# Kernel optimization log

Hardware: AMD Instinct MI355X
Metric: run time of the kernel (lower is better)

## Reference

```python
import jax, jax.numpy as jnp
import numpy as np

N, D, V = 2048, 64, 2048


def setup_inputs() -> dict:
    key = jax.random.key(0)
    k_ids, k_emb, k_tree, k_map = jax.random.split(key, 4)
    language_ids = jax.random.randint(k_ids, (N,), 0, V)
    language_embeddings = jax.random.normal(k_emb, (N, D), dtype=jnp.float32)
    # symmetric distance tables, mimicking the symmetric try/except dict lookup
    t = jax.random.uniform(k_tree, (V, V), dtype=jnp.float32)
    tree_dist = (t + t.T) * 0.5
    m = jax.random.uniform(k_map, (V, V), dtype=jnp.float32)
    map_dist = (m + m.T) * 0.5
    return {
        "language_ids": language_ids,
        "language_embeddings": language_embeddings,
        "tree_dist": tree_dist,
        "map_dist": map_dist,
    }


def reference(language_ids, language_embeddings, tree_dist, map_dist):
    # pairwise mean-L1 distance between embeddings: [N, N]
    emb_dist = jnp.mean(
        jnp.abs(language_embeddings[:, None, :] - language_embeddings[None, :, :]),
        axis=-1,
    )
    # largest_value_map_dist as computed in __init__
    largest = jnp.max(map_dist)
    ii = language_ids[:, None]  # [N, 1]
    jj = language_ids[None, :]  # [1, N]
    metric = (tree_dist[ii, jj] + map_dist[ii, jj] / largest) * 0.5  # [N, N]
    # pairs with equal language ids are skipped in the original loop
    mask = (ii != jj).astype(emb_dist.dtype)
    per_pair = jnp.abs(emb_dist - metric) * mask
    return jnp.sum(per_pair) / jnp.sum(mask)
```

## Files before the change

kernel.cpp:

```cpp
#include <hip/hip_runtime.h>
#include <hip/hip_bf16.h>

#define NL 2048
#define DE 64
#define VV 2048
#define BT 32
#define NT (NL / BT)
#define NBLK (NT * (NT + 1) / 2)
#define STA 68
#define STB 36


__global__ __launch_bounds__(1024) void prep_kernel(const int* __restrict__ ids,
                                                    const float4* __restrict__ m4,
                                                    float* __restrict__ pmax,
                                                    int* __restrict__ perm,
                                                    int* __restrict__ sids) {
    const int t = threadIdx.x;
    const int lane = t & 63, wave = t >> 6;
    const int b = blockIdx.x;

    if (b < 256) {
        const float4* p = m4 + (size_t)b * 4096;
        const float4 x0 = p[t], x1 = p[t + 1024], x2 = p[t + 2048], x3 = p[t + 3072];
        float v = fmaxf(fmaxf(fmaxf(x0.x, x0.y), fmaxf(x0.z, x0.w)),
                        fmaxf(fmaxf(x1.x, x1.y), fmaxf(x1.z, x1.w)));
        v = fmaxf(v, fmaxf(fmaxf(x2.x, x2.y), fmaxf(x2.z, x2.w)));
        v = fmaxf(v, fmaxf(fmaxf(x3.x, x3.y), fmaxf(x3.z, x3.w)));
        #pragma unroll
        for (int o = 32; o > 0; o >>= 1)
            v = fmaxf(v, __shfl_down(v, o));
        __shared__ float wl[16];
        if (lane == 0) wl[wave] = v;
        __syncthreads();
        if (t == 0) {
            float m = wl[0];
            #pragma unroll
            for (int i = 1; i < 16; ++i) m = fmaxf(m, wl[i]);
            pmax[b] = m;
        }
    } else {
        __shared__ unsigned hist[VV];
        __shared__ unsigned offs[VV];
        __shared__ unsigned wtot[16];
        __shared__ unsigned wexc[16];
        hist[2 * t] = 0u; hist[2 * t + 1] = 0u;
        __syncthreads();
        const int id0 = ids[2 * t], id1 = ids[2 * t + 1];
        atomicAdd(&hist[id0], 1u);
        atomicAdd(&hist[id1], 1u);
        __syncthreads();
        const unsigned h0 = hist[2 * t], h1 = hist[2 * t + 1];
        const unsigned s = h0 + h1;
        unsigned ps = s;
        #pragma unroll
        for (int o = 1; o < 64; o <<= 1) {
            unsigned u = __shfl_up(ps, o);
            if (lane >= o) ps += u;
        }
        if (lane == 63) wtot[wave] = ps;
        __syncthreads();
        if (wave == 0 && lane < 16) {
            unsigned v = wtot[lane];
            unsigned pv = v;
            #pragma unroll
            for (int o = 1; o < 16; o <<= 1) {
                unsigned u = __shfl_up(pv, o);
                if (lane >= o) pv += u;
            }
            wexc[lane] = pv - v;
        }
        __syncthreads();
        const unsigned ex = wexc[wave] + ps - s;
        offs[2 * t]     = ex;
        offs[2 * t + 1] = ex + h0;
        __syncthreads();
        unsigned p0 = atomicAdd(&offs[id0], 1u);
        perm[p0] = 2 * t;     sids[p0] = id0;
        unsigned p1 = atomicAdd(&offs[id1], 1u);
        perm[p1] = 2 * t + 1; sids[p1] = id1;
    }
}

__global__ __launch_bounds__(128) void loss_kernel(
    const float* __restrict__ emb,
    const float* __restrict__ tree, const float* __restrict__ mapd,
    const int* __restrict__ perm, const int* __restrict__ sids,
    const float* __restrict__ pmax,
    float* __restrict__ psum, unsigned* __restrict__ pcnt)
{
    const int t = threadIdx.x;

    const int L = blockIdx.x;
    int bi = (int)((129.0f - sqrtf(16641.0f - 8.0f * (float)L)) * 0.5f);
    if (bi > 63) bi = 63;
    while (64 * bi - bi * (bi - 1) / 2 > L) --bi;
    while (64 * (bi + 1) - (bi + 1) * bi / 2 <= L) ++bi;
    const int bj = bi + (L - (64 * bi - bi * (bi - 1) / 2));

    __shared__ __align__(16) float Ei[BT][STA];
    __shared__ __align__(16) float Ejt[DE][STB];
    __shared__ int idi[BT];
    __shared__ int idj[BT];
    __shared__ float wm[2];

    float pv = fmaxf(pmax[t], pmax[t + 128]);

    {
        const int r  = t & 31;
        const int c0 = (t >> 5) << 4;
        const int gi = perm[bi * BT + r];
        const int gj = perm[bj * BT + r];
        const float4* pa = (const float4*)(emb + (size_t)gi * DE + c0);
        const float4* pb = (const float4*)(emb + (size_t)gj * DE + c0);
        float4 a0 = pa[0], a1 = pa[1], a2 = pa[2], a3 = pa[3];
        float4 b0 = pb[0], b1 = pb[1], b2 = pb[2], b3 = pb[3];
        *(float4*)&Ei[r][c0 + 0]  = a0;
        *(float4*)&Ei[r][c0 + 4]  = a1;
        *(float4*)&Ei[r][c0 + 8]  = a2;
        *(float4*)&Ei[r][c0 + 12] = a3;
        Ejt[c0 + 0][r]  = b0.x; Ejt[c0 + 1][r]  = b0.y; Ejt[c0 + 2][r]  = b0.z; Ejt[c0 + 3][r]  = b0.w;
        Ejt[c0 + 4][r]  = b1.x; Ejt[c0 + 5][r]  = b1.y; Ejt[c0 + 6][r]  = b1.z; Ejt[c0 + 7][r]  = b1.w;
        Ejt[c0 + 8][r]  = b2.x; Ejt[c0 + 9][r]  = b2.y; Ejt[c0 + 10][r] = b2.z; Ejt[c0 + 11][r] = b2.w;
        Ejt[c0 + 12][r] = b3.x; Ejt[c0 + 13][r] = b3.y; Ejt[c0 + 14][r] = b3.z; Ejt[c0 + 15][r] = b3.w;
        if (t < BT)          idi[t] = sids[bi * BT + t];
        else if (t < 2 * BT) idj[t - BT] = sids[bj * BT + (t - BT)];
    }
    #pragma unroll
    for (int o = 32; o > 0; o >>= 1)
        pv = fmaxf(pv, __shfl_down(pv, o));
    if ((t & 63) == 0) wm[t >> 6] = pv;
    __syncthreads();

    const float inv = 1.0f / fmaxf(wm[0], wm[1]);

    const int i0 = (t >> 3) * 2;
    const int j0 = (t & 7) * 4;

    float acc[2][4];
    #pragma unroll
    for (int s = 0; s < 2; ++s)
        #pragma unroll
        for (int c = 0; c < 4; ++c) acc[s][c] = 0.0f;

    #pragma unroll 2
    for (int k = 0; k < 16; ++k) {
        float4 a0 = *(const float4*)&Ei[i0][4 * k];
        float4 a1 = *(const float4*)&Ei[i0 + 1][4 * k];
        float4 b0 = *(const float4*)&Ejt[4 * k + 0][j0];
        float4 b1 = *(const float4*)&Ejt[4 * k + 1][j0];
        float4 b2 = *(const float4*)&Ejt[4 * k + 2][j0];
        float4 b3 = *(const float4*)&Ejt[4 * k + 3][j0];
        acc[0][0] += fabsf(a0.x - b0.x) + fabsf(a0.y - b1.x) + fabsf(a0.z - b2.x) + fabsf(a0.w - b3.x);
        acc[0][1] += fabsf(a0.x - b0.y) + fabsf(a0.y - b1.y) + fabsf(a0.z - b2.y) + fabsf(a0.w - b3.y);
        acc[0][2] += fabsf(a0.x - b0.z) + fabsf(a0.y - b1.z) + fabsf(a0.z - b2.z) + fabsf(a0.w - b3.z);
        acc[0][3] += fabsf(a0.x - b0.w) + fabsf(a0.y - b1.w) + fabsf(a0.z - b2.w) + fabsf(a0.w - b3.w);
        acc[1][0] += fabsf(a1.x - b0.x) + fabsf(a1.y - b1.x) + fabsf(a1.z - b2.x) + fabsf(a1.w - b3.x);
        acc[1][1] += fabsf(a1.x - b0.y) + fabsf(a1.y - b1.y) + fabsf(a1.z - b2.y) + fabsf(a1.w - b3.y);
        acc[1][2] += fabsf(a1.x - b0.z) + fabsf(a1.y - b1.z) + fabsf(a1.z - b2.z) + fabsf(a1.w - b3.z);
        acc[1][3] += fabsf(a1.x - b0.w) + fabsf(a1.y - b1.w) + fabsf(a1.z - b2.w) + fabsf(a1.w - b3.w);
    }

    float pp = 0.0f;
    unsigned cnt = 0;
    #pragma unroll
    for (int s = 0; s < 2; ++s) {
        const int ia = idi[i0 + s];
        #pragma unroll
        for (int c = 0; c < 4; ++c) {
            const int ja = idj[j0 + c];
            const int off = ia * VV + ja;
            const float metric = (tree[off] + mapd[off] * inv) * 0.5f;
            if (ia != ja) {
                pp += fabsf(acc[s][c] * (1.0f / (float)DE) - metric);
                cnt += 1u;
            }
        }
    }

    #pragma unroll
    for (int o = 32; o > 0; o >>= 1) {
        pp  += __shfl_down(pp, o);
        cnt += __shfl_down(cnt, o);
    }
    __shared__ float    wsum_l[2];
    __shared__ unsigned wcnt_l[2];
    if ((t & 63) == 0) { wsum_l[t >> 6] = pp; wcnt_l[t >> 6] = cnt; }
    __syncthreads();
    if (t == 0) {
        const float    w = (bi == bj) ? 1.0f : 2.0f;
        const unsigned u = (bi == bj) ? 1u : 2u;
        psum[L] = (wsum_l[0] + wsum_l[1]) * w;
        pcnt[L] = (wcnt_l[0] + wcnt_l[1]) * u;
    }
}

__global__ __launch_bounds__(1024) void finalize_kernel(const float* __restrict__ psum,
                                                        const unsigned* __restrict__ pcnt,
                                                        float* __restrict__ out) {
    const int t = threadIdx.x;
    const int lane = t & 63, wave = t >> 6;
    double s = 0.0;
    unsigned c = 0;
    for (int i = t; i < NBLK; i += 1024) { s += (double)psum[i]; c += pcnt[i]; }
    #pragma unroll
    for (int o = 32; o > 0; o >>= 1) {
        s += __shfl_down(s, o);
        c += __shfl_down(c, o);
    }
    __shared__ double   sl[16];
    __shared__ unsigned cl[16];
    if (lane == 0) { sl[wave] = s; cl[wave] = c; }
    __syncthreads();
    if (t == 0) {
        double   S = sl[0];
        unsigned C = cl[0];
        #pragma unroll
        for (int i = 1; i < 16; ++i) { S += sl[i]; C += cl[i]; }
        out[0] = (float)(S / (double)C);
    }
}

extern "C" void kernel_launch(void* const* d_in, const int* in_sizes, int n_in,
                              void* d_out, int out_size, void* d_ws, size_t ws_size,
                              hipStream_t stream) {
    const int*   ids  = (const int*)d_in[0];
    const float* emb  = (const float*)d_in[1];
    const float* tree = (const float*)d_in[2];
    const float* mapd = (const float*)d_in[3];
    float* out = (float*)d_out;

    float*    pmax = (float*)d_ws;
    int*      perm = (int*)((char*)d_ws + 1024);
    int*      sids = (int*)((char*)d_ws + 9216);
    float*    psum = (float*)((char*)d_ws + 17408);
    unsigned* pcnt = (unsigned*)((char*)d_ws + 25728);

    prep_kernel<<<257, 1024, 0, stream>>>(ids, (const float4*)mapd, pmax, perm, sids);

    loss_kernel<<<NBLK, 128, 0, stream>>>(emb, tree, mapd, perm, sids, pmax, psum, pcnt);

    finalize_kernel<<<1, 1024, 0, stream>>>(psum, pcnt, out);
}
```

Before: 101.8 us.

## Enlarge loss tile to 64x64 with 4x4 register blocking per thread

Doubles the triangular tile edge from 32 to 64 and the block from 128 to 256 threads. Each thread now computes a 4x4 output micro-tile from transposed embedding tiles in shared memory, so every shared load is reused by more arithmetic. The grid shrinks from 2080 to 528 blocks, which cuts per-block index setup, pmax reduction and partial-sum overhead. The finalize kernel drops its strided loop because the block count now fits in one pass. The risk is fewer blocks for the CUs and higher register pressure per thread.

```diff
diff --git a/kernel.cpp b/kernel.cpp
--- a/kernel.cpp
+++ b/kernel.cpp
@@ -4,11 +4,10 @@
 #define NL 2048
 #define DE 64
 #define VV 2048
-#define BT 32
+#define BT 64
 #define NT (NL / BT)
 #define NBLK (NT * (NT + 1) / 2)
-#define STA 68
-#define STB 36
+#define STT 68
 
 
 __global__ __launch_bounds__(1024) void prep_kernel(const int* __restrict__ ids,
@@ -82,7 +81,7 @@
     }
 }
 
-__global__ __launch_bounds__(128) void loss_kernel(
+__global__ __launch_bounds__(256) void loss_kernel(
     const float* __restrict__ emb,
     const float* __restrict__ tree, const float* __restrict__ mapd,
     const int* __restrict__ perm, const int* __restrict__ sids,
@@ -92,33 +91,34 @@
     const int t = threadIdx.x;
 
     const int L = blockIdx.x;
-    int bi = (int)((129.0f - sqrtf(16641.0f - 8.0f * (float)L)) * 0.5f);
-    if (bi > 63) bi = 63;
-    while (64 * bi - bi * (bi - 1) / 2 > L) --bi;
-    while (64 * (bi + 1) - (bi + 1) * bi / 2 <= L) ++bi;
-    const int bj = bi + (L - (64 * bi - bi * (bi - 1) / 2));
-
-    __shared__ __align__(16) float Ei[BT][STA];
-    __shared__ __align__(16) float Ejt[DE][STB];
+    int bi = (int)((65.0f - sqrtf(4225.0f - 8.0f * (float)L)) * 0.5f);
+    if (bi > NT - 1) bi = NT - 1;
+    if (bi < 0) bi = 0;
+    while (NT * bi - bi * (bi - 1) / 2 > L) --bi;
+    while (NT * (bi + 1) - (bi + 1) * bi / 2 <= L) ++bi;
+    const int bj = bi + (L - (NT * bi - bi * (bi - 1) / 2));
+
+    __shared__ __align__(16) float Eit[DE][STT];
+    __shared__ __align__(16) float Ejt[DE][STT];
     __shared__ int idi[BT];
     __shared__ int idj[BT];
-    __shared__ float wm[2];
-
-    float pv = fmaxf(pmax[t], pmax[t + 128]);
+    __shared__ float wm[4];
+
+    float pv = pmax[t];
 
     {
-        const int r  = t & 31;
-        const int c0 = (t >> 5) << 4;
+        const int r  = t & 63;
+        const int c0 = (t >> 6) << 4;
         const int gi = perm[bi * BT + r];
         const int gj = perm[bj * BT + r];
         const float4* pa = (const float4*)(emb + (size_t)gi * DE + c0);
         const float4* pb = (const float4*)(emb + (size_t)gj * DE + c0);
         float4 a0 = pa[0], a1 = pa[1], a2 = pa[2], a3 = pa[3];
         float4 b0 = pb[0], b1 = pb[1], b2 = pb[2], b3 = pb[3];
-        *(float4*)&Ei[r][c0 + 0]  = a0;
-        *(float4*)&Ei[r][c0 + 4]  = a1;
-        *(float4*)&Ei[r][c0 + 8]  = a2;
-        *(float4*)&Ei[r][c0 + 12] = a3;
+        Eit[c0 + 0][r]  = a0.x; Eit[c0 + 1][r]  = a0.y; Eit[c0 + 2][r]  = a0.z; Eit[c0 + 3][r]  = a0.w;
+        Eit[c0 + 4][r]  = a1.x; Eit[c0 + 5][r]  = a1.y; Eit[c0 + 6][r]  = a1.z; Eit[c0 + 7][r]  = a1.w;
+        Eit[c0 + 8][r]  = a2.x; Eit[c0 + 9][r]  = a2.y; Eit[c0 + 10][r] = a2.z; Eit[c0 + 11][r] = a2.w;
+        Eit[c0 + 12][r] = a3.x; Eit[c0 + 13][r] = a3.y; Eit[c0 + 14][r] = a3.z; Eit[c0 + 15][r] = a3.w;
         Ejt[c0 + 0][r]  = b0.x; Ejt[c0 + 1][r]  = b0.y; Ejt[c0 + 2][r]  = b0.z; Ejt[c0 + 3][r]  = b0.w;
         Ejt[c0 + 4][r]  = b1.x; Ejt[c0 + 5][r]  = b1.y; Ejt[c0 + 6][r]  = b1.z; Ejt[c0 + 7][r]  = b1.w;
         Ejt[c0 + 8][r]  = b2.x; Ejt[c0 + 9][r]  = b2.y; Ejt[c0 + 10][r] = b2.z; Ejt[c0 + 11][r] = b2.w;
@@ -132,39 +132,39 @@
     if ((t & 63) == 0) wm[t >> 6] = pv;
     __syncthreads();
 
-    const float inv = 1.0f / fmaxf(wm[0], wm[1]);
-
-    const int i0 = (t >> 3) * 2;
-    const int j0 = (t & 7) * 4;
-
-    float acc[2][4];
-    #pragma unroll
-    for (int s = 0; s < 2; ++s)
+    const float inv = 1.0f / fmaxf(fmaxf(wm[0], wm[1]), fmaxf(wm[2], wm[3]));
+
+    const int i0 = (t >> 4) * 4;
+    const int j0 = (t & 15) * 4;
+
+    float acc[4][4];
+    #pragma unroll
+    for (int s = 0; s < 4; ++s)
         #pragma unroll
         for (int c = 0; c < 4; ++c) acc[s][c] = 0.0f;
 
     #pragma unroll 2
     for (int k = 0; k < 16; ++k) {
-        float4 a0 = *(const float4*)&Ei[i0][4 * k];
-        float4 a1 = *(const float4*)&Ei[i0 + 1][4 * k];
-        float4 b0 = *(const float4*)&Ejt[4 * k + 0][j0];
-        float4 b1 = *(const float4*)&Ejt[4 * k + 1][j0];
-        float4 b2 = *(const float4*)&Ejt[4 * k + 2][j0];
-        float4 b3 = *(const float4*)&Ejt[4 * k + 3][j0];
-        acc[0][0] += fabsf(a0.x - b0.x) + fabsf(a0.y - b1.x) + fabsf(a0.z - b2.x) + fabsf(a0.w - b3.x);
-        acc[0][1] += fabsf(a0.x - b0.y) + fabsf(a0.y - b1.y) + fabsf(a0.z - b2.y) + fabsf(a0.w - b3.y);
-        acc[0][2] += fabsf(a0.x - b0.z) + fabsf(a0.y - b1.z) + fabsf(a0.z - b2.z) + fabsf(a0.w - b3.z);
-        acc[0][3] += fabsf(a0.x - b0.w) + fabsf(a0.y - b1.w) + fabsf(a0.z - b2.w) + fabsf(a0.w - b3.w);
-        acc[1][0] += fabsf(a1.x - b0.x) + fabsf(a1.y - b1.x) + fabsf(a1.z - b2.x) + fabsf(a1.w - b3.x);
-        acc[1][1] += fabsf(a1.x - b0.y) + fabsf(a1.y - b1.y) + fabsf(a1.z - b2.y) + fabsf(a1.w - b3.y);
-        acc[1][2] += fabsf(a1.x - b0.z) + fabsf(a1.y - b1.z) + fabsf(a1.z - b2.z) + fabsf(a1.w - b3.z);
-        acc[1][3] += fabsf(a1.x - b0.w) + fabsf(a1.y - b1.w) + fabsf(a1.z - b2.w) + fabsf(a1.w - b3.w);
+        #pragma unroll
+        for (int q = 0; q < 4; ++q) {
+            const int d = 4 * k + q;
+            const float4 a = *(const float4*)&Eit[d][i0];
+            const float4 b = *(const float4*)&Ejt[d][j0];
+            acc[0][0] += fabsf(a.x - b.x); acc[0][1] += fabsf(a.x - b.y);
+            acc[0][2] += fabsf(a.x - b.z); acc[0][3] += fabsf(a.x - b.w);
+            acc[1][0] += fabsf(a.y - b.x); acc[1][1] += fabsf(a.y - b.y);
+            acc[1][2] += fabsf(a.y - b.z); acc[1][3] += fabsf(a.y - b.w);
+            acc[2][0] += fabsf(a.z - b.x); acc[2][1] += fabsf(a.z - b.y);
+            acc[2][2] += fabsf(a.z - b.z); acc[2][3] += fabsf(a.z - b.w);
+            acc[3][0] += fabsf(a.w - b.x); acc[3][1] += fabsf(a.w - b.y);
+            acc[3][2] += fabsf(a.w - b.z); acc[3][3] += fabsf(a.w - b.w);
+        }
     }
 
     float pp = 0.0f;
     unsigned cnt = 0;
     #pragma unroll
-    for (int s = 0; s < 2; ++s) {
+    for (int s = 0; s < 4; ++s) {
         const int ia = idi[i0 + s];
         #pragma unroll
         for (int c = 0; c < 4; ++c) {
@@ -183,15 +183,15 @@
         pp  += __shfl_down(pp, o);
         cnt += __shfl_down(cnt, o);
     }
-    __shared__ float    wsum_l[2];
-    __shared__ unsigned wcnt_l[2];
+    __shared__ float    wsum_l[4];
+    __shared__ unsigned wcnt_l[4];
     if ((t & 63) == 0) { wsum_l[t >> 6] = pp; wcnt_l[t >> 6] = cnt; }
     __syncthreads();
     if (t == 0) {
         const float    w = (bi == bj) ? 1.0f : 2.0f;
         const unsigned u = (bi == bj) ? 1u : 2u;
-        psum[L] = (wsum_l[0] + wsum_l[1]) * w;
-        pcnt[L] = (wcnt_l[0] + wcnt_l[1]) * u;
+        psum[L] = (wsum_l[0] + wsum_l[1] + wsum_l[2] + wsum_l[3]) * w;
+        pcnt[L] = (wcnt_l[0] + wcnt_l[1] + wcnt_l[2] + wcnt_l[3]) * u;
     }
 }
 
@@ -202,7 +202,7 @@
     const int lane = t & 63, wave = t >> 6;
     double s = 0.0;
     unsigned c = 0;
-    for (int i = t; i < NBLK; i += 1024) { s += (double)psum[i]; c += pcnt[i]; }
+    if (t < NBLK) { s = (double)psum[t]; c = pcnt[t]; }
     #pragma unroll
     for (int o = 32; o > 0; o >>= 1) {
         s += __shfl_down(s, o);
@@ -234,11 +234,11 @@
     int*      perm = (int*)((char*)d_ws + 1024);
     int*      sids = (int*)((char*)d_ws + 9216);
     float*    psum = (float*)((char*)d_ws + 17408);
-    unsigned* pcnt = (unsigned*)((char*)d_ws + 25728);
+    unsigned* pcnt = (unsigned*)((char*)d_ws + 19520);
 
     prep_kernel<<<257, 1024, 0, stream>>>(ids, (const float4*)mapd, pmax, perm, sids);
 
-    loss_kernel<<<NBLK, 128, 0, stream>>>(emb, tree, mapd, perm, sids, pmax, psum, pcnt);
+    loss_kernel<<<NBLK, 256, 0, stream>>>(emb, tree, mapd, perm, sids, pmax, psum, pcnt);
 
     finalize_kernel<<<1, 1024, 0, stream>>>(psum, pcnt, out);
 }
```

Measured after the change: 103.1 us. No clear change (+1.3%).
